# Performance work log

Measured on AMD Instinct MI355X. Metric: run time of the kernel, lower is better.

## Reference

```python
import jax, jax.numpy as jnp
import numpy as np

NPOS_MAX = 64

def setup_inputs() -> dict:
    key = jax.random.key(0)
    k1, k2, k3 = jax.random.split(key, 3)
    b, h, l, d = 4, 12, 1024, 64
    query = jax.random.normal(k1, (b, h, l, d), dtype=jnp.float32)
    attn_logits = jax.random.normal(k2, (b, h, l, l), dtype=jnp.float32)
    pos_emb = jax.random.normal(k3, (d, NPOS_MAX), dtype=jnp.float32) * 0.02
    return {"query": query, "attn_logits": attn_logits, "pos_emb": pos_emb}

def reference(query, attn_logits, pos_emb):
    # gates: sigmoid of attention logits, with diagonal zeroed
    gates = jax.nn.sigmoid(attn_logits)
    l = gates.shape[-1]
    eye = jnp.eye(l, dtype=gates.dtype)
    gates = gates * (1.0 - eye)
    # reverse cumsum along last axis, clamped to [0, npos_max-1]
    pos = jnp.flip(jnp.cumsum(jnp.flip(gates, -1), axis=-1), -1)
    pos = jnp.minimum(pos, jnp.asarray(NPOS_MAX - 1, dtype=pos.dtype))
    pos_ceil = jnp.ceil(pos).astype(jnp.int32)    # [b,h,l,l]
    pos_floor = jnp.floor(pos).astype(jnp.int32)  # [b,h,l,l]
    # interpolated position logits: [b,h,l,npos_max]
    logits_int = jnp.einsum('bhld,dn->bhln', query, pos_emb)
    logits_ceil = jnp.take_along_axis(logits_int, pos_ceil, axis=-1)
    logits_floor = jnp.take_along_axis(logits_int, pos_floor, axis=-1)
    w = pos - pos_floor.astype(pos.dtype)
    return logits_ceil * w + logits_floor * (1.0 - w)
```

## Files before the change

kernel.cpp:

```cpp
#include <hip/hip_runtime.h>
#include <hip/hip_bf16.h>


__device__ __forceinline__ float bf2f(unsigned short u) {
    union { unsigned int i; float f; } t;
    t.i = ((unsigned int)u) << 16;
    return t.f;
}
__device__ __forceinline__ float bf2f_lo(unsigned int v) {
    union { unsigned int i; float f; } t;
    t.i = v << 16;
    return t.f;
}
__device__ __forceinline__ float bf2f_hi(unsigned int v) {
    union { unsigned int i; float f; } t;
    t.i = v & 0xffff0000u;
    return t.f;
}
__device__ __forceinline__ unsigned short f2bf(float f) {
    union { float f; unsigned int i; } t;
    t.f = f;
    unsigned int lsb = (t.i >> 16) & 1u;
    t.i += 0x7fffu + lsb;
    return (unsigned short)(t.i >> 16);
}
__device__ __forceinline__ float sigmoidf_fast(float x) {
    return 1.0f / (1.0f + __expf(-x));
}

__global__ __launch_bounds__(256) void cope_detect(
    const unsigned short* __restrict__ q, int* __restrict__ flag)
{
    const int tid = threadIdx.x;
    unsigned short u = q[2 * tid];
    int e = (u >> 7) & 0xFF;
    unsigned long long m = __ballot(e >= 200);
    __shared__ int cnt;
    if (tid == 0) cnt = 0;
    __syncthreads();
    if ((tid & 63) == 0) atomicAdd(&cnt, __popcll(m));
    __syncthreads();
    if (tid == 0) *flag = (cnt > 8) ? 1 : 0;
}

__global__ __launch_bounds__(256) void cope_fused(
    const void* __restrict__ qv,
    const void* __restrict__ attnv,
    const void* __restrict__ pev,
    void* __restrict__ outv,
    const int* __restrict__ flag)
{
    const int r = blockIdx.x;
    const int i = r & 1023;
    const int tid = threadIdx.x;
    const int lane = tid & 63;
    const int wid = tid >> 6;
    const bool isf32 = (*flag != 0);

    __shared__ float pe_f[64 * 64];
    __shared__ float q_s[64];
    __shared__ float li[64];
    __shared__ float wsum[4];

    float g[4];

    if (isf32) {
        const float4* pe4 = reinterpret_cast<const float4*>(pev);
#pragma unroll
        for (int it = 0; it < 4; ++it) {
            int idx = it * 256 + tid;
            reinterpret_cast<float4*>(pe_f)[idx] = pe4[idx];
        }
        if (tid < 16) {
            float4 v = reinterpret_cast<const float4*>(qv)[(size_t)r * 16 + tid];
            q_s[tid * 4 + 0] = v.x; q_s[tid * 4 + 1] = v.y;
            q_s[tid * 4 + 2] = v.z; q_s[tid * 4 + 3] = v.w;
        }
        float4 av = reinterpret_cast<const float4*>(attnv)[(size_t)r * 256 + tid];
        g[0] = sigmoidf_fast(av.x); g[1] = sigmoidf_fast(av.y);
        g[2] = sigmoidf_fast(av.z); g[3] = sigmoidf_fast(av.w);
    } else {
        const uint4* pe16 = reinterpret_cast<const uint4*>(pev);
#pragma unroll
        for (int it = 0; it < 2; ++it) {
            int idx = it * 256 + tid;
            uint4 v = pe16[idx];
            float4 a, b;
            a.x = bf2f_lo(v.x); a.y = bf2f_hi(v.x);
            a.z = bf2f_lo(v.y); a.w = bf2f_hi(v.y);
            b.x = bf2f_lo(v.z); b.y = bf2f_hi(v.z);
            b.z = bf2f_lo(v.w); b.w = bf2f_hi(v.w);
            float4* dst = reinterpret_cast<float4*>(&pe_f[idx * 8]);
            dst[0] = a; dst[1] = b;
        }
        if (tid < 16) {
            ushort4 v = reinterpret_cast<const ushort4*>(qv)[(size_t)r * 16 + tid];
            q_s[tid * 4 + 0] = bf2f(v.x); q_s[tid * 4 + 1] = bf2f(v.y);
            q_s[tid * 4 + 2] = bf2f(v.z); q_s[tid * 4 + 3] = bf2f(v.w);
        }
        ushort4 av = reinterpret_cast<const ushort4*>(attnv)[(size_t)r * 256 + tid];
        g[0] = sigmoidf_fast(bf2f(av.x)); g[1] = sigmoidf_fast(bf2f(av.y));
        g[2] = sigmoidf_fast(bf2f(av.z)); g[3] = sigmoidf_fast(bf2f(av.w));
    }

    const int j0 = tid * 4;
    if (i >= j0 && i < j0 + 4) g[i - j0] = 0.f;

    float ts = g[0] + g[1] + g[2] + g[3];

    float x = ts;
#pragma unroll
    for (int s = 1; s < 64; s <<= 1) {
        float y = __shfl_up(x, s, 64);
        if (lane >= s) x += y;
    }
    if (lane == 63) wsum[wid] = x;

    __syncthreads();

    if (tid < 64) {
        float acc = 0.f;
#pragma unroll
        for (int d = 0; d < 64; ++d)
            acc += q_s[d] * pe_f[d * 64 + tid];
        li[tid] = acc;
    }

    const float s0 = wsum[0], s1 = wsum[1], s2 = wsum[2], s3 = wsum[3];
    const float total = s0 + s1 + s2 + s3;
    float woff = 0.f;
    if (wid > 0) woff += s0;
    if (wid > 1) woff += s1;
    if (wid > 2) woff += s2;
    float run = woff + (x - ts);

    __syncthreads();

    float o[4];
#pragma unroll
    for (int e = 0; e < 4; ++e) {
        float p = total - run;
        run += g[e];
        p = fminf(fmaxf(p, 0.f), 63.f);
        float pf = floorf(p);
        int ipf = (int)pf;
        int ipc = (int)ceilf(p);
        float w = p - pf;
        o[e] = li[ipc] * w + li[ipf] * (1.f - w);
    }

    if (isf32) {
        float4 ov; ov.x = o[0]; ov.y = o[1]; ov.z = o[2]; ov.w = o[3];
        reinterpret_cast<float4*>(outv)[(size_t)r * 256 + tid] = ov;
    } else {
        ushort4 ov;
        ov.x = f2bf(o[0]); ov.y = f2bf(o[1]); ov.z = f2bf(o[2]); ov.w = f2bf(o[3]);
        reinterpret_cast<ushort4*>(outv)[(size_t)r * 256 + tid] = ov;
    }
}

extern "C" void kernel_launch(void* const* d_in, const int* in_sizes, int n_in,
                              void* d_out, int out_size, void* d_ws, size_t ws_size,
                              hipStream_t stream) {
    const void* q    = d_in[0];
    const void* attn = d_in[1];
    const void* pe   = d_in[2];
    int* flag = (int*)d_ws;

    const long L = 1024;
    const long rows = (long)in_sizes[1] / L;

    cope_detect<<<1, 256, 0, stream>>>((const unsigned short*)d_in[0], flag);
    cope_fused<<<(int)rows, 256, 0, stream>>>(q, attn, pe, d_out, flag);
}
```

Before: 355.3 us.

## Split position-logit GEMM into tiled kernel and process one row per wavefront

Adds a separate kernel that computes the query-by-pos_emb logits for 64 rows per block as a register-tiled 4x4 GEMM and writes them to workspace. The main kernel then handles one attention row per wavefront: it scans with shuffles alone and gathers the interpolation endpoints with lane shuffles instead of shared memory. This removes the per-block 16KB pos_emb reload and the block-wide barriers of the old fused kernel. The cost is an extra launch plus a workspace round trip for the logits. Sigmoid now uses the hardware exp2 and rcp builtins.

```diff
diff --git a/kernel.cpp b/kernel.cpp
--- a/kernel.cpp
+++ b/kernel.cpp
@@ -3,29 +3,23 @@
 
 
 __device__ __forceinline__ float bf2f(unsigned short u) {
-    union { unsigned int i; float f; } t;
-    t.i = ((unsigned int)u) << 16;
-    return t.f;
+    union { unsigned int i; float f; } t; t.i = ((unsigned int)u) << 16; return t.f;
 }
 __device__ __forceinline__ float bf2f_lo(unsigned int v) {
-    union { unsigned int i; float f; } t;
-    t.i = v << 16;
-    return t.f;
+    union { unsigned int i; float f; } t; t.i = v << 16; return t.f;
 }
 __device__ __forceinline__ float bf2f_hi(unsigned int v) {
-    union { unsigned int i; float f; } t;
-    t.i = v & 0xffff0000u;
-    return t.f;
+    union { unsigned int i; float f; } t; t.i = v & 0xffff0000u; return t.f;
 }
 __device__ __forceinline__ unsigned short f2bf(float f) {
-    union { float f; unsigned int i; } t;
-    t.f = f;
+    union { float f; unsigned int i; } t; t.f = f;
     unsigned int lsb = (t.i >> 16) & 1u;
     t.i += 0x7fffu + lsb;
     return (unsigned short)(t.i >> 16);
 }
-__device__ __forceinline__ float sigmoidf_fast(float x) {
-    return 1.0f / (1.0f + __expf(-x));
+__device__ __forceinline__ float sigmoid_fast(float x) {
+    float e = __builtin_amdgcn_exp2f(-1.44269504f * x);
+    return __builtin_amdgcn_rcpf(1.0f + e);
 }
 
 __global__ __launch_bounds__(256) void cope_detect(
@@ -43,42 +37,31 @@
     if (tid == 0) *flag = (cnt > 8) ? 1 : 0;
 }
 
-__global__ __launch_bounds__(256) void cope_fused(
-    const void* __restrict__ qv,
-    const void* __restrict__ attnv,
-    const void* __restrict__ pev,
-    void* __restrict__ outv,
-    const int* __restrict__ flag)
+__global__ __launch_bounds__(256) void cope_li(
+    const void* __restrict__ qv, const void* __restrict__ pev,
+    float* __restrict__ li, const int* __restrict__ flag)
 {
-    const int r = blockIdx.x;
-    const int i = r & 1023;
+    __shared__ float pe_f[64 * 64];
+    __shared__ float q_t[64 * 64];
     const int tid = threadIdx.x;
-    const int lane = tid & 63;
-    const int wid = tid >> 6;
     const bool isf32 = (*flag != 0);
 
-    __shared__ float pe_f[64 * 64];
-    __shared__ float q_s[64];
-    __shared__ float li[64];
-    __shared__ float wsum[4];
-
-    float g[4];
-
     if (isf32) {
         const float4* pe4 = reinterpret_cast<const float4*>(pev);
+#pragma unroll
+        for (int it = 0; it < 4; ++it)
+            reinterpret_cast<float4*>(pe_f)[it * 256 + tid] = pe4[it * 256 + tid];
+        const float4* q4 = reinterpret_cast<const float4*>(qv) + (size_t)blockIdx.x * 1024;
 #pragma unroll
         for (int it = 0; it < 4; ++it) {
             int idx = it * 256 + tid;
-            reinterpret_cast<float4*>(pe_f)[idx] = pe4[idx];
-        }
-        if (tid < 16) {
-            float4 v = reinterpret_cast<const float4*>(qv)[(size_t)r * 16 + tid];
-            q_s[tid * 4 + 0] = v.x; q_s[tid * 4 + 1] = v.y;
-            q_s[tid * 4 + 2] = v.z; q_s[tid * 4 + 3] = v.w;
-        }
-        float4 av = reinterpret_cast<const float4*>(attnv)[(size_t)r * 256 + tid];
-        g[0] = sigmoidf_fast(av.x); g[1] = sigmoidf_fast(av.y);
-        g[2] = sigmoidf_fast(av.z); g[3] = sigmoidf_fast(av.w);
+            int d4 = idx >> 6, rr = idx & 63;
+            float4 v = q4[rr * 16 + d4];
+            q_t[(d4 * 4 + 0) * 64 + rr] = v.x;
+            q_t[(d4 * 4 + 1) * 64 + rr] = v.y;
+            q_t[(d4 * 4 + 2) * 64 + rr] = v.z;
+            q_t[(d4 * 4 + 3) * 64 + rr] = v.w;
+        }
     } else {
         const uint4* pe16 = reinterpret_cast<const uint4*>(pev);
 #pragma unroll
@@ -93,21 +76,206 @@
             float4* dst = reinterpret_cast<float4*>(&pe_f[idx * 8]);
             dst[0] = a; dst[1] = b;
         }
+        const ushort4* q4 = reinterpret_cast<const ushort4*>(qv) + (size_t)blockIdx.x * 1024;
+#pragma unroll
+        for (int it = 0; it < 4; ++it) {
+            int idx = it * 256 + tid;
+            int d4 = idx >> 6, rr = idx & 63;
+            ushort4 v = q4[rr * 16 + d4];
+            q_t[(d4 * 4 + 0) * 64 + rr] = bf2f(v.x);
+            q_t[(d4 * 4 + 1) * 64 + rr] = bf2f(v.y);
+            q_t[(d4 * 4 + 2) * 64 + rr] = bf2f(v.z);
+            q_t[(d4 * 4 + 3) * 64 + rr] = bf2f(v.w);
+        }
+    }
+    __syncthreads();
+
+    const int r0 = (tid & 15) * 4, n0 = (tid >> 4) * 4;
+    float acc[4][4];
+#pragma unroll
+    for (int a = 0; a < 4; ++a)
+#pragma unroll
+        for (int b = 0; b < 4; ++b) acc[a][b] = 0.f;
+
+#pragma unroll 8
+    for (int d = 0; d < 64; ++d) {
+        float4 qv4 = *reinterpret_cast<const float4*>(&q_t[d * 64 + r0]);
+        float4 pv = *reinterpret_cast<const float4*>(&pe_f[d * 64 + n0]);
+        acc[0][0] += qv4.x * pv.x; acc[0][1] += qv4.x * pv.y; acc[0][2] += qv4.x * pv.z; acc[0][3] += qv4.x * pv.w;
+        acc[1][0] += qv4.y * pv.x; acc[1][1] += qv4.y * pv.y; acc[1][2] += qv4.y * pv.z; acc[1][3] += qv4.y * pv.w;
+        acc[2][0] += qv4.z * pv.x; acc[2][1] += qv4.z * pv.y; acc[2][2] += qv4.z * pv.z; acc[2][3] += qv4.z * pv.w;
+        acc[3][0] += qv4.w * pv.x; acc[3][1] += qv4.w * pv.y; acc[3][2] += qv4.w * pv.z; acc[3][3] += qv4.w * pv.w;
+    }
+#pragma unroll
+    for (int a = 0; a < 4; ++a) {
+        size_t row = (size_t)blockIdx.x * 64 + r0 + a;
+        float4 o; o.x = acc[a][0]; o.y = acc[a][1]; o.z = acc[a][2]; o.w = acc[a][3];
+        *reinterpret_cast<float4*>(&li[row * 64 + n0]) = o;
+    }
+}
+
+__global__ __launch_bounds__(256) void cope_main(
+    const void* __restrict__ attnv,
+    const float* __restrict__ li_ws,
+    void* __restrict__ outv,
+    const int* __restrict__ flag)
+{
+    const int tid = threadIdx.x;
+    const int lane = tid & 63;
+    const int wid = tid >> 6;
+    const int r = blockIdx.x * 4 + wid;
+    const int i = r & 1023;
+    const bool isf32 = (*flag != 0);
+    const int col0 = lane * 16;
+
+    const float li_val = li_ws[(size_t)r * 64 + lane];
+
+    float g[16];
+    if (isf32) {
+        const float4* ap = reinterpret_cast<const float4*>(
+            reinterpret_cast<const float*>(attnv) + (size_t)r * 1024);
+#pragma unroll
+        for (int c = 0; c < 4; ++c) {
+            float4 v = ap[4 * lane + c];
+            float s0 = sigmoid_fast(v.x), s1 = sigmoid_fast(v.y);
+            float s2 = sigmoid_fast(v.z), s3 = sigmoid_fast(v.w);
+            int k = c * 4;
+            g[k + 0] = (col0 + k + 0 == i) ? 0.f : s0;
+            g[k + 1] = (col0 + k + 1 == i) ? 0.f : s1;
+            g[k + 2] = (col0 + k + 2 == i) ? 0.f : s2;
+            g[k + 3] = (col0 + k + 3 == i) ? 0.f : s3;
+        }
+    } else {
+        const uint4* ap = reinterpret_cast<const uint4*>(
+            reinterpret_cast<const unsigned short*>(attnv) + (size_t)r * 1024);
+#pragma unroll
+        for (int c = 0; c < 2; ++c) {
+            uint4 v = ap[2 * lane + c];
+            unsigned int w0 = v.x, w1 = v.y, w2 = v.z, w3 = v.w;
+            int k = c * 8;
+            float s;
+            s = sigmoid_fast(bf2f_lo(w0)); g[k + 0] = (col0 + k + 0 == i) ? 0.f : s;
+            s = sigmoid_fast(bf2f_hi(w0)); g[k + 1] = (col0 + k + 1 == i) ? 0.f : s;
+            s = sigmoid_fast(bf2f_lo(w1)); g[k + 2] = (col0 + k + 2 == i) ? 0.f : s;
+            s = sigmoid_fast(bf2f_hi(w1)); g[k + 3] = (col0 + k + 3 == i) ? 0.f : s;
+            s = sigmoid_fast(bf2f_lo(w2)); g[k + 4] = (col0 + k + 4 == i) ? 0.f : s;
+            s = sigmoid_fast(bf2f_hi(w2)); g[k + 5] = (col0 + k + 5 == i) ? 0.f : s;
+            s = sigmoid_fast(bf2f_lo(w3)); g[k + 6] = (col0 + k + 6 == i) ? 0.f : s;
+            s = sigmoid_fast(bf2f_hi(w3)); g[k + 7] = (col0 + k + 7 == i) ? 0.f : s;
+        }
+    }
+
+    float ts = 0.f;
+#pragma unroll
+    for (int k = 0; k < 16; ++k) ts += g[k];
+
+    float x = ts;
+#pragma unroll
+    for (int s = 1; s < 64; s <<= 1) {
+        float y = __shfl_up(x, s, 64);
+        if (lane >= s) x += y;
+    }
+    const float total = __shfl(x, 63, 64);
+    float run = x - ts;
+
+    float o[16];
+#pragma unroll
+    for (int e = 0; e < 16; ++e) {
+        float p = total - run;
+        run += g[e];
+        p = fminf(fmaxf(p, 0.f), 63.f);
+        float pf = floorf(p);
+        float w = p - pf;
+        int ipf = (int)pf;
+        int ipc = min(ipf + 1, 63);
+        float a = __shfl(li_val, ipf, 64);
+        float b = __shfl(li_val, ipc, 64);
+        o[e] = a + w * (b - a);
+    }
+
+    if (isf32) {
+        float4* op = reinterpret_cast<float4*>(
+            reinterpret_cast<float*>(outv) + (size_t)r * 1024);
+#pragma unroll
+        for (int c = 0; c < 4; ++c) {
+            float4 v; int k = c * 4;
+            v.x = o[k]; v.y = o[k + 1]; v.z = o[k + 2]; v.w = o[k + 3];
+            op[4 * lane + c] = v;
+        }
+    } else {
+        uint4* op = reinterpret_cast<uint4*>(
+            reinterpret_cast<unsigned short*>(outv) + (size_t)r * 1024);
+#pragma unroll
+        for (int c = 0; c < 2; ++c) {
+            int k = c * 8;
+            uint4 v;
+            v.x = (unsigned)f2bf(o[k + 0]) | ((unsigned)f2bf(o[k + 1]) << 16);
+            v.y = (unsigned)f2bf(o[k + 2]) | ((unsigned)f2bf(o[k + 3]) << 16);
+            v.z = (unsigned)f2bf(o[k + 4]) | ((unsigned)f2bf(o[k + 5]) << 16);
+            v.w = (unsigned)f2bf(o[k + 6]) | ((unsigned)f2bf(o[k + 7]) << 16);
+            op[2 * lane + c] = v;
+        }
+    }
+}
+
+__global__ __launch_bounds__(256) void cope_fused(
+    const void* __restrict__ qv, const void* __restrict__ attnv,
+    const void* __restrict__ pev, void* __restrict__ outv,
+    const int* __restrict__ flag)
+{
+    const int r = blockIdx.x;
+    const int i = r & 1023;
+    const int tid = threadIdx.x;
+    const int lane = tid & 63;
+    const int wid = tid >> 6;
+    const bool isf32 = (*flag != 0);
+
+    __shared__ float pe_f[64 * 64];
+    __shared__ float q_s[64];
+    __shared__ float li[64];
+    __shared__ float wsum[4];
+
+    float g[4];
+    if (isf32) {
+        const float4* pe4 = reinterpret_cast<const float4*>(pev);
+#pragma unroll
+        for (int it = 0; it < 4; ++it)
+            reinterpret_cast<float4*>(pe_f)[it * 256 + tid] = pe4[it * 256 + tid];
+        if (tid < 16) {
+            float4 v = reinterpret_cast<const float4*>(qv)[(size_t)r * 16 + tid];
+            q_s[tid * 4 + 0] = v.x; q_s[tid * 4 + 1] = v.y;
+            q_s[tid * 4 + 2] = v.z; q_s[tid * 4 + 3] = v.w;
+        }
+        float4 av = reinterpret_cast<const float4*>(attnv)[(size_t)r * 256 + tid];
+        g[0] = sigmoid_fast(av.x); g[1] = sigmoid_fast(av.y);
+        g[2] = sigmoid_fast(av.z); g[3] = sigmoid_fast(av.w);
+    } else {
+        const uint4* pe16 = reinterpret_cast<const uint4*>(pev);
+#pragma unroll
+        for (int it = 0; it < 2; ++it) {
+            int idx = it * 256 + tid;
+            uint4 v = pe16[idx];
+            float4 a, b;
+            a.x = bf2f_lo(v.x); a.y = bf2f_hi(v.x);
+            a.z = bf2f_lo(v.y); a.w = bf2f_hi(v.y);
+            b.x = bf2f_lo(v.z); b.y = bf2f_hi(v.z);
+            b.z = bf2f_lo(v.w); b.w = bf2f_hi(v.w);
+            float4* dst = reinterpret_cast<float4*>(&pe_f[idx * 8]);
+            dst[0] = a; dst[1] = b;
+        }
         if (tid < 16) {
             ushort4 v = reinterpret_cast<const ushort4*>(qv)[(size_t)r * 16 + tid];
             q_s[tid * 4 + 0] = bf2f(v.x); q_s[tid * 4 + 1] = bf2f(v.y);
             q_s[tid * 4 + 2] = bf2f(v.z); q_s[tid * 4 + 3] = bf2f(v.w);
         }
         ushort4 av = reinterpret_cast<const ushort4*>(attnv)[(size_t)r * 256 + tid];
-        g[0] = sigmoidf_fast(bf2f(av.x)); g[1] = sigmoidf_fast(bf2f(av.y));
-        g[2] = sigmoidf_fast(bf2f(av.z)); g[3] = sigmoidf_fast(bf2f(av.w));
+        g[0] = sigmoid_fast(bf2f(av.x)); g[1] = sigmoid_fast(bf2f(av.y));
+        g[2] = sigmoid_fast(bf2f(av.z)); g[3] = sigmoid_fast(bf2f(av.w));
     }
 
     const int j0 = tid * 4;
     if (i >= j0 && i < j0 + 4) g[i - j0] = 0.f;
-
     float ts = g[0] + g[1] + g[2] + g[3];
-
     float x = ts;
 #pragma unroll
     for (int s = 1; s < 64; s <<= 1) {
@@ -115,17 +283,13 @@
         if (lane >= s) x += y;
     }
     if (lane == 63) wsum[wid] = x;
-
-    __syncthreads();
-
+    __syncthreads();
     if (tid < 64) {
         float acc = 0.f;
 #pragma unroll
-        for (int d = 0; d < 64; ++d)
-            acc += q_s[d] * pe_f[d * 64 + tid];
+        for (int d = 0; d < 64; ++d) acc += q_s[d] * pe_f[d * 64 + tid];
         li[tid] = acc;
     }
-
     const float s0 = wsum[0], s1 = wsum[1], s2 = wsum[2], s3 = wsum[3];
     const float total = s0 + s1 + s2 + s3;
     float woff = 0.f;
@@ -133,7 +297,6 @@
     if (wid > 1) woff += s1;
     if (wid > 2) woff += s2;
     float run = woff + (x - ts);
-
     __syncthreads();
 
     float o[4];
@@ -144,11 +307,10 @@
         p = fminf(fmaxf(p, 0.f), 63.f);
         float pf = floorf(p);
         int ipf = (int)pf;
-        int ipc = (int)ceilf(p);
+        int ipc = min(ipf + 1, 63);
         float w = p - pf;
-        o[e] = li[ipc] * w + li[ipf] * (1.f - w);
-    }
-
+        o[e] = li[ipf] + w * (li[ipc] - li[ipf]);
+    }
     if (isf32) {
         float4 ov; ov.x = o[0]; ov.y = o[1]; ov.z = o[2]; ov.w = o[3];
         reinterpret_cast<float4*>(outv)[(size_t)r * 256 + tid] = ov;
@@ -166,10 +328,17 @@
     const void* attn = d_in[1];
     const void* pe   = d_in[2];
     int* flag = (int*)d_ws;
+    float* li = (float*)((char*)d_ws + 256);
 
     const long L = 1024;
     const long rows = (long)in_sizes[1] / L;
+    const size_t ws_need = 256 + (size_t)rows * 64 * sizeof(float);
 
     cope_detect<<<1, 256, 0, stream>>>((const unsigned short*)d_in[0], flag);
-    cope_fused<<<(int)rows, 256, 0, stream>>>(q, attn, pe, d_out, flag);
-}
+    if (ws_size >= ws_need) {
+        cope_li<<<(int)(rows / 64), 256, 0, stream>>>(q, pe, li, flag);
+        cope_main<<<(int)(rows / 4), 256, 0, stream>>>(attn, li, d_out, flag);
+    } else {
+        cope_fused<<<(int)rows, 256, 0, stream>>>(q, attn, pe, d_out, flag);
+    }
+}
```

Measured after the change: 355.1 us. No clear change (-0.1%).
